# Kernel optimization log

Hardware: AMD Instinct MI355X
Metric: run time of the kernel (lower is better)

Reference implementation:

```python
import jax, jax.numpy as jnp
import numpy as np

B, S, D = 4, 2048, 2048
H = 16
NOPE, ROPE, VD = 128, 64, 128
QK = NOPE + ROPE            # 192 per-head q/k dim
KVR = 512                   # kv_lora_rank
THETA = 10000.0
EPS = 1e-6
SCALE = QK ** -0.5


def _freqs(seq_len, d, theta):
    inv = 1.0 / (theta ** (np.arange(0, d, 2, dtype=np.float64) / d))
    ang = np.outer(np.arange(seq_len, dtype=np.float64), inv)  # [S, d//2]
    return jnp.asarray(np.cos(ang), jnp.float32), jnp.asarray(np.sin(ang), jnp.float32)


def apply_rope(x, cos, sin):
    # x: [B, S, H, d]; cos/sin: [S, d//2]; complex multiply on (even, odd) pairs
    xr = x.reshape(*x.shape[:-1], -1, 2)
    xe, xo = xr[..., 0], xr[..., 1]
    c = cos[None, :, None, :]
    s = sin[None, :, None, :]
    ye = xe * c - xo * s
    yo = xe * s + xo * c
    return jnp.stack([ye, yo], axis=-1).reshape(x.shape)


def rmsnorm(x, w, eps=EPS):
    return x * jax.lax.rsqrt(jnp.mean(x * x, axis=-1, keepdims=True) + eps) * w


def setup_inputs() -> dict:
    key = jax.random.key(0)
    ks = jax.random.split(key, 6)
    sd = 0.02
    x = jax.random.normal(ks[0], (B, S, D), jnp.float32)
    wq = jax.random.normal(ks[1], (H * QK, D), jnp.float32) * sd
    wkv_a = jax.random.normal(ks[2], (KVR + ROPE, D), jnp.float32) * sd
    kv_norm_w = jnp.ones((KVR,), jnp.float32)
    wkv_b = jax.random.normal(ks[3], (H * (NOPE + VD), KVR), jnp.float32) * sd
    wo = jax.random.normal(ks[4], (D, H * VD), jnp.float32) * sd
    cos, sin = _freqs(S, ROPE, THETA)
    return {"x": x, "wq": wq, "wkv_a": wkv_a, "kv_norm_w": kv_norm_w,
            "wkv_b": wkv_b, "wo": wo, "freqs_cos": cos, "freqs_sin": sin}


def reference(x, wq, wkv_a, kv_norm_w, wkv_b, wo, freqs_cos, freqs_sin):
    b, s, _ = x.shape
    # query projection (q_lora_rank == 0 path)
    q = jnp.einsum('bsd,ed->bse', x, wq).reshape(b, s, H, QK)
    q_nope, q_pe = q[..., :NOPE], q[..., NOPE:]
    q_pe = apply_rope(q_pe, freqs_cos, freqs_sin)

    # low-rank KV latent + decoupled rope key
    kv = jnp.einsum('bsd,ed->bse', x, wkv_a)          # [b,s,KVR+ROPE]
    kv_c, k_pe = kv[..., :KVR], kv[..., KVR:]
    k_pe = apply_rope(k_pe[:, :, None, :], freqs_cos, freqs_sin)  # [b,s,1,ROPE]
    kv_c = rmsnorm(kv_c, kv_norm_w)
    kvb = jnp.einsum('bsr,er->bse', kv_c, wkv_b).reshape(b, s, H, NOPE + VD)
    k_nope, v = kvb[..., :NOPE], kvb[..., NOPE:]
    k = jnp.concatenate([k_nope, jnp.broadcast_to(k_pe, (b, s, H, ROPE))], axis=-1)
    q_full = jnp.concatenate([q_nope, q_pe], axis=-1)

    # causal attention
    scores = jnp.einsum('bqhd,bkhd->bhqk', q_full, k) * SCALE
    mask = jnp.triu(jnp.full((s, s), -jnp.inf, jnp.float32), k=1)
    scores = scores + mask[None, None]
    p = jax.nn.softmax(scores, axis=-1)
    out = jnp.einsum('bhqk,bkhd->bqhd', p, v).reshape(b, s, H * VD)
    return jnp.einsum('bse,de->bsd', out, wo)
```

## Files before the change

### kernel.cpp

```cpp
#include <hip/hip_runtime.h>
#include <math.h>

#define BB 4
#define SS 2048
#define DD 2048
#define HH 16
#define NOPE 128
#define ROPE 64
#define VD 128
#define QKD 192
#define KVR 512
#define NP1 3712
#define ROWS (BB*SS)
#define SCL2 0.1041216338380858f

typedef __attribute__((ext_vector_type(8))) short bf16x8;
typedef __attribute__((ext_vector_type(4))) float f32x4;
typedef unsigned short bfu;
typedef __attribute__((address_space(1))) const void GV;
typedef __attribute__((address_space(3))) void LV;

__device__ __forceinline__ float bf2f(unsigned int u) {
    unsigned int i = u << 16; float f; __builtin_memcpy(&f, &i, 4); return f;
}
__device__ __forceinline__ unsigned int f2bf(float f) {
    unsigned int i; __builtin_memcpy(&i, &f, 4);
    return (i + 0x7fffu + ((i >> 16) & 1u)) >> 16;
}
__device__ __forceinline__ unsigned int cvt_pk_bf16(float lo, float hi) {
    unsigned int r;
    asm("v_cvt_pk_bf16_f32 %0, %1, %2" : "=v"(r) : "v"(lo), "v"(hi));
    return r;
}

__global__ void cast_f32_bf16(const float* __restrict__ src, bfu* __restrict__ dst,
                              long n_src, long n_dst) {
    long i = (long)blockIdx.x * blockDim.x + threadIdx.x;
    if (i * 4 >= n_dst) return;
    unsigned int lo = 0, hi = 0;
    if (i * 4 < n_src) {
        float4 v = ((const float4*)src)[i];
        lo = f2bf(v.x) | (f2bf(v.y) << 16);
        hi = f2bf(v.z) | (f2bf(v.w) << 16);
    }
    ((uint2*)dst)[i] = make_uint2(lo, hi);
}

__global__ void cast_weights(const float* __restrict__ wq, const float* __restrict__ wa,
                             const float* __restrict__ wb, const float* __restrict__ wo,
                             bfu* __restrict__ dq, bfu* __restrict__ da,
                             bfu* __restrict__ db, bfu* __restrict__ dwo) {
    long i = (long)blockIdx.x * 256 + threadIdx.x;
    const float* src; bfu* dst; long off, n_src; float scl = 1.0f;
    if (i < 1572864L)        { src = wq; dst = dq;  off = i;            n_src = 1572864L; scl = SCL2; }
    else if (i < 1900544L)   { src = wa; dst = da;  off = i - 1572864L; n_src = 294912L;  }
    else if (i < 2424832L)   { src = wb; dst = db;  off = i - 1900544L; n_src = 524288L;  }
    else if (i < 3473408L)   { src = wo; dst = dwo; off = i - 2424832L; n_src = 1048576L; }
    else return;
    unsigned int lo = 0, hi = 0;
    if (off < n_src) {
        float4 v = ((const float4*)src)[off];
        lo = f2bf(v.x * scl) | (f2bf(v.y * scl) << 16);
        hi = f2bf(v.z * scl) | (f2bf(v.w * scl) << 16);
    }
    ((uint2*)dst)[off] = make_uint2(lo, hi);
}

template <int MODE>
__global__ void __launch_bounds__(256)
gemm_bt(const bfu* __restrict__ A, const bfu* __restrict__ Bt,
        void* __restrict__ Cv, bfu* __restrict__ C2, int N, int K) {
    __shared__ __align__(16) char lds[32768];
    char* AsB = lds;
    char* BsB = lds + 16384;
    const int tid  = threadIdx.x;
    const int lane = tid & 63;
    const int wid  = tid >> 6;
    const int wr   = wid >> 1, wc = wid & 1;
    const int nwg  = gridDim.x * gridDim.y;
    const int flat = blockIdx.y * gridDim.x + blockIdx.x;
    const int swz  = (flat & 7) * (nwg >> 3) + (flat >> 3);
    const long m0 = (long)(swz / gridDim.x) * 128;
    const long n0 = (long)(swz % gridDim.x) * 128;

    f32x4 acc[4][4] = {};

    const int lr = lane >> 3;
    const int SB = (lane & 7) << 4;

    for (int k0 = 0; k0 < K; k0 += 64) {
        __syncthreads();
#pragma unroll
        for (int i = 0; i < 4; ++i) {
            int rb = wid * 32 + i * 8;
            int R  = rb + lr;
            int c  = (SB ^ ((R & 7) << 4)) >> 1;
            const bfu* gA = A  + (m0 + R) * (long)K + k0 + c;
            const bfu* gB = Bt + (n0 + R) * (long)K + k0 + c;
            __builtin_amdgcn_global_load_lds((GV*)gA, (LV*)(AsB + rb * 128), 16, 0, 0);
            __builtin_amdgcn_global_load_lds((GV*)gB, (LV*)(BsB + rb * 128), 16, 0, 0);
        }
        __syncthreads();
#pragma unroll
        for (int kk = 0; kk < 2; ++kk) {
            bf16x8 av[4], bv[4];
            const int cb = kk * 64 + ((lane >> 4) << 4);
#pragma unroll
            for (int m = 0; m < 4; ++m) {
                int R = wr * 64 + m * 16 + (lane & 15);
                av[m] = *(const bf16x8*)(AsB + R * 128 + (cb ^ ((R & 7) << 4)));
            }
#pragma unroll
            for (int n = 0; n < 4; ++n) {
                int R = wc * 64 + n * 16 + (lane & 15);
                bv[n] = *(const bf16x8*)(BsB + R * 128 + (cb ^ ((R & 7) << 4)));
            }
#pragma unroll
            for (int m = 0; m < 4; ++m)
#pragma unroll
                for (int n = 0; n < 4; ++n)
                    acc[m][n] = __builtin_amdgcn_mfma_f32_16x16x32_bf16(av[m], bv[n], acc[m][n], 0, 0, 0);
        }
    }

    const int cr = (lane >> 4) << 2;
    const int cc = lane & 15;
#pragma unroll
    for (int m = 0; m < 4; ++m)
#pragma unroll
        for (int n = 0; n < 4; ++n)
#pragma unroll
            for (int r = 0; r < 4; ++r) {
                long row = m0 + wr * 64 + m * 16 + cr + r;
                long col = n0 + wc * 64 + n * 16 + cc;
                float val = acc[m][n][r];
                if (MODE == 1) {
                    ((float*)Cv)[row * N + col] = val;
                } else if (MODE == 2) {
                    long b_ = row >> 11;
                    long s  = row & 2047;
                    long h  = col >> 8;
                    long wi = col & 255;
                    if (wi < 128)
                        C2[((b_ * HH + h) * SS + s) * (long)QKD + wi] = (bfu)f2bf(val);
                    else
                        ((bfu*)Cv)[row * 2048 + h * 128 + (wi - 128)] = (bfu)f2bf(val);
                } else {
                    long b_ = row >> 11;
                    long s  = row & 2047;
                    if (col < 3072) {
                        unsigned int h = (unsigned int)col / 192u;
                        unsigned int d = (unsigned int)col - h * 192u;
                        ((bfu*)Cv)[((b_ * HH + h) * SS + s) * (long)QKD + d] = (bfu)f2bf(val);
                    } else {
                        C2[row * 640 + (col - 3072)] = (bfu)f2bf(val);
                    }
                }
            }
}

__global__ void rope_pe_fill(bfu* __restrict__ qr, const bfu* __restrict__ kpe,
                             bfu* __restrict__ kall,
                             const float* __restrict__ fc, const float* __restrict__ fs) {
    long t = (long)blockIdx.x * 256 + threadIdx.x;
    int  ch = (int)(t & 7);
    long r  = t >> 3;
    int  s  = (int)(r & 2047);
    long bh = (r >> 11) & 63;
    long b_ = bh >> 4;
    if (t < 1048576L) {
        bfu* p = qr + (bh * SS + s) * (long)QKD + NOPE + ch * 8;
        bf16x8 v = *(const bf16x8*)p;
        int i0 = ch * 4;
        unsigned int out[4];
#pragma unroll
        for (int k = 0; k < 4; ++k) {
            float e = bf2f((unsigned short)v[2 * k]);
            float o = bf2f((unsigned short)v[2 * k + 1]);
            float c = fc[s * 32 + i0 + k], sn = fs[s * 32 + i0 + k];
            out[k] = cvt_pk_bf16(e * c - o * sn, e * sn + o * c);
        }
        *(uint4*)p = make_uint4(out[0], out[1], out[2], out[3]);
    } else {
        bf16x8 v = *(const bf16x8*)(kpe + (b_ * SS + s) * (long)ROPE + ch * 8);
        *(bf16x8*)(kall + (bh * SS + s) * (long)QKD + NOPE + ch * 8) = v;
    }
}

__global__ void __launch_bounds__(256)
rms_rope_kv(const bfu* __restrict__ kv1, const float* __restrict__ wn,
            bfu* __restrict__ kvc, bfu* __restrict__ kpe,
            const float* __restrict__ fc, const float* __restrict__ fs) {
    const int row = blockIdx.x;
    const int t   = threadIdx.x;
    const int s   = row & (SS - 1);
    const long base = (long)row * 640;
    unsigned int v = *(const unsigned int*)(kv1 + base + 2 * t);
    float a = bf2f(v & 0xffff), c2 = bf2f(v >> 16);
    float ssum = a * a + c2 * c2;
#pragma unroll
    for (int d = 1; d < 64; d <<= 1) ssum += __shfl_xor(ssum, d);
    __shared__ float red[4];
    const int lane = t & 63, w = t >> 6;
    if (lane == 0) red[w] = ssum;
    __syncthreads();
    float tot = red[0] + red[1] + red[2] + red[3];
    float scale = rsqrtf(tot * (1.0f / 512.0f) + 1e-6f);
    float w0 = wn[2 * t], w1 = wn[2 * t + 1];
    unsigned int out = f2bf(a * scale * w0) | (f2bf(c2 * scale * w1) << 16);
    *(unsigned int*)(kvc + (long)row * KVR + 2 * t) = out;
    if (t < 32) {
        unsigned int pv = *(const unsigned int*)(kv1 + base + KVR + 2 * t);
        float e = bf2f(pv & 0xffff), o = bf2f(pv >> 16);
        float cc = fc[s * 32 + t], sn = fs[s * 32 + t];
        unsigned int po = f2bf(e * cc - o * sn) | (f2bf(e * sn + o * cc) << 16);
        *(unsigned int*)(kpe + (long)row * ROPE + 2 * t) = po;
    }
}

__global__ void __launch_bounds__(256)
transpose_v2(const bfu* __restrict__ vpack, bfu* __restrict__ vt) {
    __shared__ __align__(16) char tile[64 * 256];
    const int tid = threadIdx.x;
    const int bid = blockIdx.x;
    const int st  = bid & 31;
    const int bh  = bid >> 5;
    const int h   = bh & 15;
    const long b_ = bh >> 4;
    const long sbase = b_ * SS + st * 64;
#pragma unroll
    for (int i = 0; i < 4; ++i) {
        int idx = i * 256 + tid;
        int row = idx >> 4;
        int ch  = (idx & 15) ^ ((row >> 3) & 7);
        const bfu* src = vpack + (sbase + row) * 2048 + h * 128 + ch * 8;
        __builtin_amdgcn_global_load_lds((GV*)src, (LV*)(tile + idx * 16), 16, 0, 0);
    }
    __syncthreads();
#pragma unroll
    for (int i = 0; i < 4; ++i) {
        int idx = i * 256 + tid;
        int sc = idx & 7;
        int v  = (idx >> 3) & 127;
        bfu tmp[8];
#pragma unroll
        for (int k = 0; k < 8; ++k) {
            int row = sc * 8 + k;
            tmp[k] = *(const bfu*)(tile + row * 256 + (((v >> 3) ^ ((row >> 3) & 7)) << 4) + (v & 7) * 2);
        }
        *(bf16x8*)(vt + ((long)bh * VD + v) * SS + st * 64 + sc * 8) = *(bf16x8*)tmp;
    }
}

template <bool MASKED>
__device__ __forceinline__ void attn_tile64(
    const char* kbuf, const char* vbuf, char* pw,
    const bf16x8 (&qf)[6], f32x4 (&accv)[8],
    float& ms, float& ls, int kv0, int qa, int ql, int kg, int lane) {
    f32x4 sc[4] = {};
#pragma unroll
    for (int j = 0; j < 4; ++j)
#pragma unroll
        for (int d = 0; d < 6; ++d) {
            int row  = j * 16 + ql;
            int slot = (d * 4 + kg) ^ (ql & 7);
            bf16x8 kf = *(const bf16x8*)(kbuf + row * 384 + slot * 16);
            sc[j] = __builtin_amdgcn_mfma_f32_16x16x32_bf16(kf, qf[d], sc[j], 0, 0, 0);
        }
    float p[4][4];
    float mx = -1e30f;
#pragma unroll
    for (int j = 0; j < 4; ++j)
#pragma unroll
        for (int r = 0; r < 4; ++r) {
            float s = sc[j][r];
            if (MASKED) {
                int kv = kv0 + j * 16 + kg * 4 + r;
                s = (kv > qa) ? -1e30f : s;
            }
            p[j][r] = s;
            mx = fmaxf(mx, s);
        }
    mx = fmaxf(mx, __shfl_xor(mx, 16));
    mx = fmaxf(mx, __shfl_xor(mx, 32));
    float rs = 0.f;
    if (__all(mx <= ms)) {
#pragma unroll
        for (int j = 0; j < 4; ++j)
#pragma unroll
            for (int r = 0; r < 4; ++r) {
                float e = exp2f(p[j][r] - ms);
                p[j][r] = e;
                rs += e;
            }
        rs += __shfl_xor(rs, 16);
        rs += __shfl_xor(rs, 32);
        ls += rs;
    } else {
        float mn = fmaxf(ms, mx);
        float al = exp2f(ms - mn);
        ms = mn;
#pragma unroll
        for (int j = 0; j < 4; ++j)
#pragma unroll
            for (int r = 0; r < 4; ++r) {
                float e = exp2f(p[j][r] - mn);
                p[j][r] = e;
                rs += e;
            }
        rs += __shfl_xor(rs, 16);
        rs += __shfl_xor(rs, 32);
        ls = ls * al + rs;
        float alT[4];
#pragma unroll
        for (int r = 0; r < 4; ++r)
            alT[r] = __shfl(al, (lane & 48) + kg * 4 + r);
#pragma unroll
        for (int v8 = 0; v8 < 8; ++v8)
#pragma unroll
            for (int r = 0; r < 4; ++r)
                accv[v8][r] *= alT[r];
    }
#pragma unroll
    for (int j = 0; j < 4; ++j) {
        uint2 u;
        u.x = cvt_pk_bf16(p[j][0], p[j][1]);
        u.y = cvt_pk_bf16(p[j][2], p[j][3]);
        int slot = (2 * j + (kg >> 1)) ^ (ql & 7);
        *(uint2*)(pw + ql * 128 + slot * 16 + (kg & 1) * 8) = u;
    }
    asm volatile("s_waitcnt lgkmcnt(0)" ::: "memory");
#pragma unroll
    for (int t2 = 0; t2 < 2; ++t2) {
        int ps = (t2 * 4 + kg) ^ (ql & 7);
        bf16x8 pa = *(const bf16x8*)(pw + ql * 128 + ps * 16);
#pragma unroll
        for (int v8 = 0; v8 < 8; ++v8) {
            int vrow = v8 * 16 + ql;
            int vs   = (t2 * 4 + kg) ^ (ql & 7);
            bf16x8 vf = *(const bf16x8*)(vbuf + vrow * 128 + vs * 16);
            accv[v8] = __builtin_amdgcn_mfma_f32_16x16x32_bf16(pa, vf, accv[v8], 0, 0, 0);
        }
    }
}

__global__ void __launch_bounds__(512)
attn(const bfu* __restrict__ qr, const bfu* __restrict__ kall,
     const bfu* __restrict__ vt, bfu* __restrict__ ao) {
    __shared__ __align__(16) char kbuf[64 * 384];
    __shared__ __align__(16) char vbuf[128 * 128];
    __shared__ __align__(16) char pbuf[8][2048];
    const int tid  = threadIdx.x;
    const int lane = tid & 63;
    const int w    = tid >> 6;
    const int ql   = lane & 15;
    const int kg   = lane >> 4;
    const int bid  = blockIdx.x;
    const int qb   = 15 - (bid >> 6);
    const int bh   = bid & 63;
    const int h    = bh & 15;
    const int b    = bh >> 4;
    const char* Q  = (const char*)(qr + (long)bh * SS * QKD);
    const char* Kp = (const char*)(kall + (long)bh * SS * QKD);
    const char* Vp = (const char*)(vt + (long)bh * VD * SS);
    char* pw = pbuf[w];

    const int qa_min = qb * 128 + w * 16;
    const int qa = qa_min + ql;

    bf16x8 qf[6];
#pragma unroll
    for (int d = 0; d < 6; ++d)
        qf[d] = *(const bf16x8*)(Q + (long)(qa_min + ql) * 384 + d * 64 + kg * 16);

    f32x4 accv[8] = {};
    float ms = -1e30f, ls = 0.f;
    const int ntiles = 2 * qb + 2;

    for (int t = 0; t < ntiles; ++t) {
        const int kv0 = t * 64;
        __syncthreads();
#pragma unroll
        for (int i = 0; i < 3; ++i) {
            int idx  = i * 512 + tid;
            int row  = idx / 24;
            int slot = idx - row * 24;
            int ss   = slot ^ (row & 7);
            const char* src = Kp + (long)(kv0 + row) * 384 + ss * 16;
            __builtin_amdgcn_global_load_lds((GV*)src, (LV*)(kbuf + idx * 16), 16, 0, 0);
        }
#pragma unroll
        for (int i = 0; i < 2; ++i) {
            int idx  = i * 512 + tid;
            int row  = idx >> 3;
            int slot = idx & 7;
            int ss   = slot ^ (row & 7);
            const char* src = Vp + (long)row * (SS * 2) + kv0 * 2 + ss * 16;
            __builtin_amdgcn_global_load_lds((GV*)src, (LV*)(vbuf + idx * 16), 16, 0, 0);
        }
        __syncthreads();
        if (kv0 + 63 <= qa_min)
            attn_tile64<false>(kbuf, vbuf, pw, qf, accv, ms, ls, kv0, qa, ql, kg, lane);
        else if (kv0 <= qa_min + 15)
            attn_tile64<true>(kbuf, vbuf, pw, qf, accv, ms, ls, kv0, qa, ql, kg, lane);
    }
    float li[4];
#pragma unroll
    for (int r = 0; r < 4; ++r)
        li[r] = 1.0f / __shfl(ls, (lane & 48) + kg * 4 + r);
#pragma unroll
    for (int v8 = 0; v8 < 8; ++v8)
#pragma unroll
        for (int r = 0; r < 4; ++r) {
            float o = accv[v8][r] * li[r];
            long row = (long)b * SS + qa_min + kg * 4 + r;
            ao[row * (long)(HH * VD) + h * VD + v8 * 16 + ql] = (bfu)f2bf(o);
        }
}

#define O_XB   0L
#define O_WQ   33554432L
#define O_WA   46137344L
#define O_WB   48758784L
#define O_WO   52953088L
#define O_KALL 61341696L
#define O_KV1  111673344L
#define O_QR   122159104L
#define O_KVC  172490752L
#define O_KPE  180879360L
#define O_AO   181927936L
#define WS_NEED 215482368L

extern "C" void kernel_launch(void* const* d_in, const int* in_sizes, int n_in,
                              void* d_out, int out_size, void* d_ws, size_t ws_size,
                              hipStream_t stream) {
    const float* x      = (const float*)d_in[0];
    const float* wq     = (const float*)d_in[1];
    const float* wkv_a  = (const float*)d_in[2];
    const float* kvnw   = (const float*)d_in[3];
    const float* wkv_b  = (const float*)d_in[4];
    const float* wo     = (const float*)d_in[5];
    const float* fcos   = (const float*)d_in[6];
    const float* fsin   = (const float*)d_in[7];
    if (ws_size < (size_t)WS_NEED) return;

    char* ws = (char*)d_ws;
    bfu* xb   = (bfu*)(ws + O_XB);
    bfu* wqb  = (bfu*)(ws + O_WQ);
    bfu* wbb  = (bfu*)(ws + O_WB);
    bfu* wob  = (bfu*)(ws + O_WO);
    bfu* kall = (bfu*)(ws + O_KALL);
    bfu* kv1  = (bfu*)(ws + O_KV1);
    bfu* qr   = (bfu*)(ws + O_QR);
    bfu* kvc  = (bfu*)(ws + O_KVC);
    bfu* kpe  = (bfu*)(ws + O_KPE);
    bfu* ao   = (bfu*)(ws + O_AO);
    bfu* wab  = (bfu*)(ws + O_WA);
    bfu* vt   = xb;
    bfu* vpack = (bfu*)d_out;

    cast_f32_bf16<<<16384, 256, 0, stream>>>(x, xb, 16777216L, 16777216L);
    cast_weights<<<13568, 256, 0, stream>>>(wq, wkv_a, wkv_b, wo, wqb, wab, wbb, wob);

    gemm_bt<3><<<dim3(29, 64), 256, 0, stream>>>(xb, wqb, qr, kv1, NP1, DD);

    rms_rope_kv<<<ROWS, 256, 0, stream>>>(kv1, kvnw, kvc, kpe, fcos, fsin);

    gemm_bt<2><<<dim3(32, 64), 256, 0, stream>>>(kvc, wbb, vpack, kall, HH * 256, KVR);

    rope_pe_fill<<<8192, 256, 0, stream>>>(qr, kpe, kall, fcos, fsin);
    transpose_v2<<<2048, 256, 0, stream>>>(vpack, vt);

    attn<<<1024, 512, 0, stream>>>(qr, kall, vt, ao);

    gemm_bt<1><<<dim3(16, 64), 256, 0, stream>>>(ao, wob, d_out, nullptr, DD, HH * VD);
}
```

Baseline: 511.7 us.

## Register-prefetch next K/V tile in attention and merge cast kernels

```diff
diff --git a/kernel.cpp b/kernel.cpp
--- a/kernel.cpp
+++ b/kernel.cpp
@@ -33,29 +33,19 @@
     return r;
 }
 
-__global__ void cast_f32_bf16(const float* __restrict__ src, bfu* __restrict__ dst,
-                              long n_src, long n_dst) {
-    long i = (long)blockIdx.x * blockDim.x + threadIdx.x;
-    if (i * 4 >= n_dst) return;
-    unsigned int lo = 0, hi = 0;
-    if (i * 4 < n_src) {
-        float4 v = ((const float4*)src)[i];
-        lo = f2bf(v.x) | (f2bf(v.y) << 16);
-        hi = f2bf(v.z) | (f2bf(v.w) << 16);
-    }
-    ((uint2*)dst)[i] = make_uint2(lo, hi);
-}
-
-__global__ void cast_weights(const float* __restrict__ wq, const float* __restrict__ wa,
-                             const float* __restrict__ wb, const float* __restrict__ wo,
-                             bfu* __restrict__ dq, bfu* __restrict__ da,
-                             bfu* __restrict__ db, bfu* __restrict__ dwo) {
+__global__ void cast_all(const float* __restrict__ x, const float* __restrict__ wq,
+                         const float* __restrict__ wa, const float* __restrict__ wb,
+                         const float* __restrict__ wo,
+                         bfu* __restrict__ dx, bfu* __restrict__ dq,
+                         bfu* __restrict__ da, bfu* __restrict__ db,
+                         bfu* __restrict__ dwo) {
     long i = (long)blockIdx.x * 256 + threadIdx.x;
     const float* src; bfu* dst; long off, n_src; float scl = 1.0f;
-    if (i < 1572864L)        { src = wq; dst = dq;  off = i;            n_src = 1572864L; scl = SCL2; }
-    else if (i < 1900544L)   { src = wa; dst = da;  off = i - 1572864L; n_src = 294912L;  }
-    else if (i < 2424832L)   { src = wb; dst = db;  off = i - 1900544L; n_src = 524288L;  }
-    else if (i < 3473408L)   { src = wo; dst = dwo; off = i - 2424832L; n_src = 1048576L; }
+    if (i < 4194304L)        { src = x;  dst = dx;  off = i;            n_src = 4194304L; }
+    else if (i < 5767168L)   { src = wq; dst = dq;  off = i - 4194304L; n_src = 1572864L; scl = SCL2; }
+    else if (i < 6094848L)   { src = wa; dst = da;  off = i - 5767168L; n_src = 294912L;  }
+    else if (i < 6619136L)   { src = wb; dst = db;  off = i - 6094848L; n_src = 524288L;  }
+    else if (i < 7667712L)   { src = wo; dst = dwo; off = i - 6619136L; n_src = 1048576L; }
     else return;
     unsigned int lo = 0, hi = 0;
     if (off < n_src) {
@@ -368,6 +358,27 @@
     const int qa_min = qb * 128 + w * 16;
     const int qa = qa_min + ql;
 
+    const char* ksrc[3]; int kdst[3];
+#pragma unroll
+    for (int i = 0; i < 3; ++i) {
+        int idx  = i * 512 + tid;
+        int row  = idx / 24;
+        int slot = idx - row * 24;
+        int ss   = slot ^ (row & 7);
+        ksrc[i]  = Kp + (long)row * 384 + ss * 16;
+        kdst[i]  = idx * 16;
+    }
+    const char* vsrc[2]; int vdst[2];
+#pragma unroll
+    for (int i = 0; i < 2; ++i) {
+        int idx  = i * 512 + tid;
+        int row  = idx >> 3;
+        int slot = idx & 7;
+        int ss   = slot ^ (row & 7);
+        vsrc[i]  = Vp + (long)row * (SS * 2) + ss * 16;
+        vdst[i]  = idx * 16;
+    }
+
     bf16x8 qf[6];
 #pragma unroll
     for (int d = 0; d < 6; ++d)
@@ -377,28 +388,28 @@
     float ms = -1e30f, ls = 0.f;
     const int ntiles = 2 * qb + 2;
 
+    uint4 kreg[3], vreg[2];
+#pragma unroll
+    for (int i = 0; i < 3; ++i) kreg[i] = *(const uint4*)(ksrc[i]);
+#pragma unroll
+    for (int i = 0; i < 2; ++i) vreg[i] = *(const uint4*)(vsrc[i]);
+
     for (int t = 0; t < ntiles; ++t) {
         const int kv0 = t * 64;
         __syncthreads();
 #pragma unroll
-        for (int i = 0; i < 3; ++i) {
-            int idx  = i * 512 + tid;
-            int row  = idx / 24;
-            int slot = idx - row * 24;
-            int ss   = slot ^ (row & 7);
-            const char* src = Kp + (long)(kv0 + row) * 384 + ss * 16;
-            __builtin_amdgcn_global_load_lds((GV*)src, (LV*)(kbuf + idx * 16), 16, 0, 0);
-        }
-#pragma unroll
-        for (int i = 0; i < 2; ++i) {
-            int idx  = i * 512 + tid;
-            int row  = idx >> 3;
-            int slot = idx & 7;
-            int ss   = slot ^ (row & 7);
-            const char* src = Vp + (long)row * (SS * 2) + kv0 * 2 + ss * 16;
-            __builtin_amdgcn_global_load_lds((GV*)src, (LV*)(vbuf + idx * 16), 16, 0, 0);
-        }
+        for (int i = 0; i < 3; ++i) *(uint4*)(kbuf + kdst[i]) = kreg[i];
+#pragma unroll
+        for (int i = 0; i < 2; ++i) *(uint4*)(vbuf + vdst[i]) = vreg[i];
         __syncthreads();
+        if (t + 1 < ntiles) {
+            const long ko = (long)(kv0 + 64) * 384;
+            const long vo = (long)(kv0 + 64) * 2;
+#pragma unroll
+            for (int i = 0; i < 3; ++i) kreg[i] = *(const uint4*)(ksrc[i] + ko);
+#pragma unroll
+            for (int i = 0; i < 2; ++i) vreg[i] = *(const uint4*)(vsrc[i] + vo);
+        }
         if (kv0 + 63 <= qa_min)
             attn_tile64<false>(kbuf, vbuf, pw, qf, accv, ms, ls, kv0, qa, ql, kg, lane);
         else if (kv0 <= qa_min + 15)
@@ -447,6 +458,7 @@
     char* ws = (char*)d_ws;
     bfu* xb   = (bfu*)(ws + O_XB);
     bfu* wqb  = (bfu*)(ws + O_WQ);
+    bfu* wab  = (bfu*)(ws + O_WA);
     bfu* wbb  = (bfu*)(ws + O_WB);
     bfu* wob  = (bfu*)(ws + O_WO);
     bfu* kall = (bfu*)(ws + O_KALL);
@@ -455,12 +467,10 @@
     bfu* kvc  = (bfu*)(ws + O_KVC);
     bfu* kpe  = (bfu*)(ws + O_KPE);
     bfu* ao   = (bfu*)(ws + O_AO);
-    bfu* wab  = (bfu*)(ws + O_WA);
     bfu* vt   = xb;
     bfu* vpack = (bfu*)d_out;
 
-    cast_f32_bf16<<<16384, 256, 0, stream>>>(x, xb, 16777216L, 16777216L);
-    cast_weights<<<13568, 256, 0, stream>>>(wq, wkv_a, wkv_b, wo, wqb, wab, wbb, wob);
+    cast_all<<<29952, 256, 0, stream>>>(x, wq, wkv_a, wkv_b, wo, xb, wqb, wab, wbb, wob);
 
     gemm_bt<3><<<dim3(29, 64), 256, 0, stream>>>(xb, wqb, qr, kv1, NP1, DD);
 
```

After: 564.1 us. 10.2% more time.

## Double-buffer K/V tiles in attention to overlap loads with compute

Applied to the files above, without the earlier changes.

```diff
diff --git a/kernel.cpp b/kernel.cpp
--- a/kernel.cpp
+++ b/kernel.cpp
@@ -347,8 +347,8 @@
 __global__ void __launch_bounds__(512)
 attn(const bfu* __restrict__ qr, const bfu* __restrict__ kall,
      const bfu* __restrict__ vt, bfu* __restrict__ ao) {
-    __shared__ __align__(16) char kbuf[64 * 384];
-    __shared__ __align__(16) char vbuf[128 * 128];
+    __shared__ __align__(16) char kbuf[2][64 * 384];
+    __shared__ __align__(16) char vbuf[2][128 * 128];
     __shared__ __align__(16) char pbuf[8][2048];
     const int tid  = threadIdx.x;
     const int lane = tid & 63;
@@ -368,6 +368,37 @@
     const int qa_min = qb * 128 + w * 16;
     const int qa = qa_min + ql;
 
+    const char* ksrc[3]; int kdst[3];
+#pragma unroll
+    for (int i = 0; i < 3; ++i) {
+        int idx  = i * 512 + tid;
+        int row  = idx / 24;
+        int slot = idx - row * 24;
+        int ss   = slot ^ (row & 7);
+        ksrc[i]  = Kp + (long)row * 384 + ss * 16;
+        kdst[i]  = idx * 16;
+    }
+    const char* vsrc[2]; int vdst[2];
+#pragma unroll
+    for (int i = 0; i < 2; ++i) {
+        int idx  = i * 512 + tid;
+        int row  = idx >> 3;
+        int slot = idx & 7;
+        int ss   = slot ^ (row & 7);
+        vsrc[i]  = Vp + (long)row * (SS * 2) + ss * 16;
+        vdst[i]  = idx * 16;
+    }
+    auto stage = [&](int bi, int kv0) {
+        const long ko = (long)kv0 * 384;
+        const long vo = (long)kv0 * 2;
+#pragma unroll
+        for (int i = 0; i < 3; ++i)
+            __builtin_amdgcn_global_load_lds((GV*)(ksrc[i] + ko), (LV*)(kbuf[bi] + kdst[i]), 16, 0, 0);
+#pragma unroll
+        for (int i = 0; i < 2; ++i)
+            __builtin_amdgcn_global_load_lds((GV*)(vsrc[i] + vo), (LV*)(vbuf[bi] + vdst[i]), 16, 0, 0);
+    };
+
     bf16x8 qf[6];
 #pragma unroll
     for (int d = 0; d < 6; ++d)
@@ -377,32 +408,21 @@
     float ms = -1e30f, ls = 0.f;
     const int ntiles = 2 * qb + 2;
 
+    stage(0, 0);
+    __syncthreads();
+
     for (int t = 0; t < ntiles; ++t) {
+        const int cur = t & 1;
         const int kv0 = t * 64;
-        __syncthreads();
-#pragma unroll
-        for (int i = 0; i < 3; ++i) {
-            int idx  = i * 512 + tid;
-            int row  = idx / 24;
-            int slot = idx - row * 24;
-            int ss   = slot ^ (row & 7);
-            const char* src = Kp + (long)(kv0 + row) * 384 + ss * 16;
-            __builtin_amdgcn_global_load_lds((GV*)src, (LV*)(kbuf + idx * 16), 16, 0, 0);
-        }
-#pragma unroll
-        for (int i = 0; i < 2; ++i) {
-            int idx  = i * 512 + tid;
-            int row  = idx >> 3;
-            int slot = idx & 7;
-            int ss   = slot ^ (row & 7);
-            const char* src = Vp + (long)row * (SS * 2) + kv0 * 2 + ss * 16;
-            __builtin_amdgcn_global_load_lds((GV*)src, (LV*)(vbuf + idx * 16), 16, 0, 0);
-        }
-        __syncthreads();
+        if (t + 1 < ntiles)
+            stage(cur ^ 1, kv0 + 64);
         if (kv0 + 63 <= qa_min)
-            attn_tile64<false>(kbuf, vbuf, pw, qf, accv, ms, ls, kv0, qa, ql, kg, lane);
+            attn_tile64<false>(kbuf[cur], vbuf[cur], pw, qf, accv, ms, ls, kv0, qa, ql, kg, lane);
         else if (kv0 <= qa_min + 15)
-            attn_tile64<true>(kbuf, vbuf, pw, qf, accv, ms, ls, kv0, qa, ql, kg, lane);
+            attn_tile64<true>(kbuf[cur], vbuf[cur], pw, qf, accv, ms, ls, kv0, qa, ql, kg, lane);
+        asm volatile("s_waitcnt vmcnt(0)" ::: "memory");
+        __builtin_amdgcn_s_barrier();
+        asm volatile("" ::: "memory");
     }
     float li[4];
 #pragma unroll
@@ -447,6 +467,7 @@
     char* ws = (char*)d_ws;
     bfu* xb   = (bfu*)(ws + O_XB);
     bfu* wqb  = (bfu*)(ws + O_WQ);
+    bfu* wab  = (bfu*)(ws + O_WA);
     bfu* wbb  = (bfu*)(ws + O_WB);
     bfu* wob  = (bfu*)(ws + O_WO);
     bfu* kall = (bfu*)(ws + O_KALL);
@@ -455,7 +476,6 @@
     bfu* kvc  = (bfu*)(ws + O_KVC);
     bfu* kpe  = (bfu*)(ws + O_KPE);
     bfu* ao   = (bfu*)(ws + O_AO);
-    bfu* wab  = (bfu*)(ws + O_WA);
     bfu* vt   = xb;
     bfu* vpack = (bfu*)d_out;
 
```

After: 508.2 us. About the same (-0.7%).
